# Optimization experiments

Hardware: AMD Instinct MI355X
Metric: run time of the kernel (lower is better)

The kernel has to match this reference:

```python
import jax, jax.numpy as jnp
import numpy as np

DIM = 512
NUM_HEADS = 8
B, NW, W = 8, 64, 64  # batch, num_windows, window_size


def setup_inputs() -> dict:
    key = jax.random.key(0)
    k1, k2, k3 = jax.random.split(key, 3)
    x = jax.random.normal(k1, (B, NW, W, DIM), dtype=jnp.float32)
    w_qkv = jax.random.normal(k2, (DIM, 3 * DIM), dtype=jnp.float32) * (DIM ** -0.5)
    w_proj = jax.random.normal(k3, (DIM, DIM), dtype=jnp.float32) * (DIM ** -0.5)
    b_proj = jnp.zeros((DIM,), dtype=jnp.float32)
    return {"x": x, "w_qkv": w_qkv, "w_proj": w_proj, "b_proj": b_proj}


def reference(x, w_qkv, w_proj, b_proj):
    batch, nw, w, dim = x.shape
    heads = NUM_HEADS
    dh = dim // heads
    scale = dh ** -0.5
    # qkv projection (no bias): [B, nW, W, 3*dim]
    qkv = jnp.einsum('bnwc,cd->bnwd', x, w_qkv)
    # -> [B, nW, W, 3, H, dh] -> [3, B, H, nW, W, dh]
    qkv = qkv.reshape(batch, nw, w, 3, heads, dh)
    qkv = jnp.transpose(qkv, (3, 0, 4, 1, 2, 5))
    q, k, v = qkv[0], qkv[1], qkv[2]
    # attention logits per window: [B, H, nW, W, W]
    attn = jnp.einsum('bhnqd,bhnkd->bhnqk', q, k) * scale
    attn = jax.nn.softmax(attn, axis=-1)
    # [B, H, nW, W, dh]
    out = jnp.einsum('bhnqk,bhnkd->bhnqd', attn, v)
    # faithful raw reshape (no transpose), matching the TF source
    out = out.reshape(batch, nw, w, dim)
    return jnp.einsum('bnwc,cd->bnwd', out, w_proj) + b_proj
```

## Files before the change

kernel.cpp:

```cpp
#include <hip/hip_runtime.h>
#include <hip/hip_bf16.h>

typedef __bf16 bf16_t;
typedef __bf16 bf16x8 __attribute__((ext_vector_type(8)));
typedef float f32x4 __attribute__((ext_vector_type(4)));

__global__ __launch_bounds__(256) void transpose_cast_kernel(
    const float* __restrict__ src, bf16_t* __restrict__ dst, int R, int C)
{
    __shared__ float tile[32][33];
    const int bx = blockIdx.x;
    const int by = blockIdx.y;
    const int t  = threadIdx.x;
    const int i0 = t >> 5;
    const int j  = t & 31;
#pragma unroll
    for (int p = 0; p < 4; ++p) {
        int i = i0 + p * 8;
        tile[i][j] = src[(long)(by * 32 + i) * C + bx * 32 + j];
    }
    __syncthreads();
#pragma unroll
    for (int p = 0; p < 4; ++p) {
        int i = i0 + p * 8;
        dst[(long)(bx * 32 + i) * R + by * 32 + j] = (bf16_t)tile[j][i];
    }
}

__global__ __launch_bounds__(256) void qkv_attn_kernel(
    const float*  __restrict__ x,
    const bf16_t* __restrict__ wT,
    bf16_t* __restrict__ ao)
{
    __shared__ bf16_t arena1[64 * 72];
    __shared__ bf16_t arena2[192 * 72];

    bf16_t* const lXc = arena1;
    bf16_t* const lP  = arena1;
    bf16_t* const lW  = arena2;
    bf16_t* const lQ  = arena2;
    bf16_t* const lK  = arena2 + 64 * 72;
    bf16_t* const lVT = arena2 + 128 * 72;

    const int id  = blockIdx.x;
    const int xcd = id & 7;
    const int s   = id >> 3;
    const int wid = xcd * 64 + (s >> 3);
    const int h   = s & 7;

    const int bb  = wid >> 6;
    const int nw  = wid & 63;
    const float* xw = x + (long)wid * 64 * 512;

    const int t    = threadIdx.x;
    const int wave = t >> 6;
    const int lane = t & 63;
    const int lr   = lane & 15;
    const int q    = lane >> 4;

    const float scale = 0.125f;

    f32x4 acc[12];
#pragma unroll
    for (int j = 0; j < 12; ++j) acc[j] = (f32x4)0.0f;

    for (int kc = 0; kc < 8; ++kc) {
        const int k0 = kc * 64;
#pragma unroll
        for (int p = 0; p < 2; ++p) {
            const int v = t + p * 256;
            const int r = v >> 3, c = (v & 7) * 8;
            const float* rp = xw + (long)r * 512 + k0 + c;
            f32x4 f0 = *(const f32x4*)rp;
            f32x4 f1 = *(const f32x4*)(rp + 4);
            bf16x8 o;
            o[0] = (bf16_t)f0[0]; o[1] = (bf16_t)f0[1];
            o[2] = (bf16_t)f0[2]; o[3] = (bf16_t)f0[3];
            o[4] = (bf16_t)f1[0]; o[5] = (bf16_t)f1[1];
            o[6] = (bf16_t)f1[2]; o[7] = (bf16_t)f1[3];
            *(bf16x8*)&lXc[r * 72 + c] = o;
        }
#pragma unroll
        for (int p = 0; p < 6; ++p) {
            const int v = t + p * 256;
            const int nr = v >> 3, c = (v & 7) * 8;
            const int g = nr >> 6, i = nr & 63;
            *(bf16x8*)&lW[nr * 72 + c] =
                *(const bf16x8*)(wT + (long)(g * 512 + h * 64 + i) * 512 + k0 + c);
        }
        __syncthreads();
#pragma unroll
        for (int ks = 0; ks < 64; ks += 32) {
            bf16x8 af = *(const bf16x8*)&lXc[(wave * 16 + lr) * 72 + ks + q * 8];
#pragma unroll
            for (int j = 0; j < 12; ++j) {
                bf16x8 bf = *(const bf16x8*)&lW[(j * 16 + lr) * 72 + ks + q * 8];
                acc[j] = __builtin_amdgcn_mfma_f32_16x16x32_bf16(af, bf, acc[j], 0, 0, 0);
            }
        }
        __syncthreads();
    }

#pragma unroll
    for (int j = 0; j < 4; ++j)
#pragma unroll
        for (int reg = 0; reg < 4; ++reg) {
            const int row = wave * 16 + q * 4 + reg;
            lQ[row * 72 + j * 16 + lr] = (bf16_t)acc[j][reg];
        }
#pragma unroll
    for (int j = 4; j < 8; ++j)
#pragma unroll
        for (int reg = 0; reg < 4; ++reg) {
            const int row = wave * 16 + q * 4 + reg;
            lK[row * 72 + (j - 4) * 16 + lr] = (bf16_t)acc[j][reg];
        }
#pragma unroll
    for (int j = 8; j < 12; ++j)
#pragma unroll
        for (int reg = 0; reg < 4; ++reg) {
            const int row = wave * 16 + q * 4 + reg;
            lVT[((j - 8) * 16 + lr) * 72 + row] = (bf16_t)acc[j][reg];
        }
    __syncthreads();

    f32x4 sAcc[4];
#pragma unroll
    for (int j = 0; j < 4; ++j) sAcc[j] = (f32x4)0.0f;
#pragma unroll
    for (int ks = 0; ks < 64; ks += 32) {
        bf16x8 aq = *(const bf16x8*)&lQ[(wave * 16 + lr) * 72 + ks + q * 8];
#pragma unroll
        for (int j = 0; j < 4; ++j) {
            bf16x8 bk = *(const bf16x8*)&lK[(j * 16 + lr) * 72 + ks + q * 8];
            sAcc[j] = __builtin_amdgcn_mfma_f32_16x16x32_bf16(aq, bk, sAcc[j], 0, 0, 0);
        }
    }

#pragma unroll
    for (int reg = 0; reg < 4; ++reg) {
        float m = fmaxf(fmaxf(sAcc[0][reg], sAcc[1][reg]),
                        fmaxf(sAcc[2][reg], sAcc[3][reg]));
#pragma unroll
        for (int d = 1; d < 16; d <<= 1) m = fmaxf(m, __shfl_xor(m, d));
        float p[4];
        float sum = 0.0f;
#pragma unroll
        for (int j = 0; j < 4; ++j) {
            p[j] = __expf((sAcc[j][reg] - m) * scale);
            sum += p[j];
        }
#pragma unroll
        for (int d = 1; d < 16; d <<= 1) sum += __shfl_xor(sum, d);
        const float inv = 1.0f / sum;
        const int row = wave * 16 + q * 4 + reg;
#pragma unroll
        for (int j = 0; j < 4; ++j)
            lP[row * 72 + j * 16 + lr] = (bf16_t)(p[j] * inv);
    }

    f32x4 o[4];
#pragma unroll
    for (int d4 = 0; d4 < 4; ++d4) o[d4] = (f32x4)0.0f;
#pragma unroll
    for (int ks = 0; ks < 64; ks += 32) {
        bf16x8 ap = *(const bf16x8*)&lP[(wave * 16 + lr) * 72 + ks + q * 8];
#pragma unroll
        for (int d4 = 0; d4 < 4; ++d4) {
            bf16x8 bv = *(const bf16x8*)&lVT[(d4 * 16 + lr) * 72 + ks + q * 8];
            o[d4] = __builtin_amdgcn_mfma_f32_16x16x32_bf16(ap, bv, o[d4], 0, 0, 0);
        }
    }

    bf16_t* aop = ao + ((long)bb * 4096 + (long)h * 512 + nw * 8) * 512;
#pragma unroll
    for (int d4 = 0; d4 < 4; ++d4)
#pragma unroll
        for (int reg = 0; reg < 4; ++reg) {
            const int wr = wave * 16 + q * 4 + reg;
            aop[(long)(wr >> 3) * 512 + (wr & 7) * 64 + d4 * 16 + lr] =
                (bf16_t)o[d4][reg];
        }
}

#define LDP 72

__global__ __launch_bounds__(256) void gemm2_kernel(
    const bf16_t* __restrict__ A,
    const bf16_t* __restrict__ Bt,
    const float*  __restrict__ bias,
    float* __restrict__ C,
    int M, int N, int K)
{
    __shared__ bf16_t lA[128 * LDP];
    __shared__ bf16_t lB[128 * LDP];

    const int tid  = threadIdx.x;
    const int wave = tid >> 6;
    const int lane = tid & 63;
    const int wm   = wave >> 1;
    const int wn   = wave & 1;
    const int lr   = lane & 15;
    const int q    = lane >> 4;

    const int id  = blockIdx.x;
    const int xcd = id & 7;
    const int s   = id >> 3;
    const int bm  = xcd * 32 + (s >> 2);
    const int bn  = s & 3;

    const long arow0 = (long)bm * 128;
    const long brow0 = (long)bn * 128;

    f32x4 acc[4][4];
#pragma unroll
    for (int i = 0; i < 4; ++i)
#pragma unroll
        for (int j = 0; j < 4; ++j) acc[i][j] = (f32x4)0.0f;

    const int srow = tid >> 3;
    const int scol = (tid & 7) * 8;

    const int nk = K / 64;
    for (int kt = 0; kt < nk; ++kt) {
        const bf16_t* Ag = A + arow0 * K + kt * 64;
        const bf16_t* Bg = Bt + brow0 * K + kt * 64;
        bf16x8 av[4], bv[4];
#pragma unroll
        for (int p = 0; p < 4; ++p) {
            const int r = srow + p * 32;
            av[p] = *(const bf16x8*)(Ag + (long)r * K + scol);
            bv[p] = *(const bf16x8*)(Bg + (long)r * K + scol);
        }
#pragma unroll
        for (int p = 0; p < 4; ++p) {
            const int r = srow + p * 32;
            *(bf16x8*)&lA[r * LDP + scol] = av[p];
            *(bf16x8*)&lB[r * LDP + scol] = bv[p];
        }
        __syncthreads();
#pragma unroll
        for (int ks = 0; ks < 64; ks += 32) {
            bf16x8 af[4], bf[4];
#pragma unroll
            for (int i = 0; i < 4; ++i)
                af[i] = *(const bf16x8*)&lA[(wm * 64 + i * 16 + lr) * LDP + ks + q * 8];
#pragma unroll
            for (int j = 0; j < 4; ++j)
                bf[j] = *(const bf16x8*)&lB[(wn * 64 + j * 16 + lr) * LDP + ks + q * 8];
#pragma unroll
            for (int i = 0; i < 4; ++i)
#pragma unroll
                for (int j = 0; j < 4; ++j)
                    acc[i][j] = __builtin_amdgcn_mfma_f32_16x16x32_bf16(
                        af[i], bf[j], acc[i][j], 0, 0, 0);
        }
        __syncthreads();
    }

#pragma unroll
    for (int i = 0; i < 4; ++i) {
        const long r = arow0 + wm * 64 + i * 16 + q * 4;
#pragma unroll
        for (int j = 0; j < 4; ++j) {
            const long c = brow0 + wn * 64 + j * 16 + lr;
            const float bv2 = bias[c];
#pragma unroll
            for (int reg = 0; reg < 4; ++reg) {
                C[(r + reg) * N + c] = acc[i][j][reg] + bv2;
            }
        }
    }
}

extern "C" void kernel_launch(void* const* d_in, const int* in_sizes, int n_in,
                              void* d_out, int out_size, void* d_ws, size_t ws_size,
                              hipStream_t stream)
{
    (void)in_sizes; (void)n_in; (void)out_size; (void)ws_size;
    const float* x     = (const float*)d_in[0];
    const float* wqkv  = (const float*)d_in[1];
    const float* wproj = (const float*)d_in[2];
    const float* bproj = (const float*)d_in[3];
    float* out = (float*)d_out;

    bf16_t* wT = (bf16_t*)d_ws;
    bf16_t* pT = wT + (size_t)1536 * 512;
    bf16_t* ao = pT + (size_t)512 * 512;

    transpose_cast_kernel<<<dim3(48, 16), 256, 0, stream>>>(wqkv, wT, 512, 1536);
    transpose_cast_kernel<<<dim3(16, 16), 256, 0, stream>>>(wproj, pT, 512, 512);

    qkv_attn_kernel<<<4096, 256, 0, stream>>>(x, wT, ao);

    gemm2_kernel<<<1024, 256, 0, stream>>>(
        ao, pT, bproj, out, 32768, 512, 512);
}
```

Before: 228.9 us.

## Process two windows per block with 2x2 wave tiling and pre-cast x to bf16

Each block of the fused QKV+attention kernel now handles two windows (128 rows) instead of one, with waves arranged 2x2 so each wave computes a 64x96 sub-tile of the QKV projection. This reuses each loaded weight tile across twice as many rows, halving weight traffic per window. x is cast to bf16 once by a separate elementwise kernel, so the fused kernel loads bf16 directly. LDS padding is removed (stride 64), which may add bank conflicts. The extra cast pass adds a full read and write of x, and launch bounds now request 3 blocks per CU.

```diff
diff --git a/kernel.cpp b/kernel.cpp
--- a/kernel.cpp
+++ b/kernel.cpp
@@ -27,160 +27,201 @@
     }
 }
 
-__global__ __launch_bounds__(256) void qkv_attn_kernel(
-    const float*  __restrict__ x,
+__global__ __launch_bounds__(256) void cast_bf16_kernel(
+    const float* __restrict__ src, bf16_t* __restrict__ dst, long n)
+{
+    const long i = ((long)blockIdx.x * 256 + threadIdx.x) * 8;
+    if (i < n) {
+        f32x4 a = *(const f32x4*)(src + i);
+        f32x4 b = *(const f32x4*)(src + i + 4);
+        bf16x8 o;
+        o[0] = (bf16_t)a[0]; o[1] = (bf16_t)a[1];
+        o[2] = (bf16_t)a[2]; o[3] = (bf16_t)a[3];
+        o[4] = (bf16_t)b[0]; o[5] = (bf16_t)b[1];
+        o[6] = (bf16_t)b[2]; o[7] = (bf16_t)b[3];
+        *(bf16x8*)(dst + i) = o;
+    }
+}
+
+__global__ __launch_bounds__(256, 3) void qkv_attn_kernel(
+    const bf16_t* __restrict__ xb,
     const bf16_t* __restrict__ wT,
     bf16_t* __restrict__ ao)
 {
-    __shared__ bf16_t arena1[64 * 72];
-    __shared__ bf16_t arena2[192 * 72];
-
-    bf16_t* const lXc = arena1;
-    bf16_t* const lP  = arena1;
-    bf16_t* const lW  = arena2;
-    bf16_t* const lQ  = arena2;
-    bf16_t* const lK  = arena2 + 64 * 72;
-    bf16_t* const lVT = arena2 + 128 * 72;
-
-    const int id  = blockIdx.x;
-    const int xcd = id & 7;
-    const int s   = id >> 3;
-    const int wid = xcd * 64 + (s >> 3);
-    const int h   = s & 7;
-
-    const int bb  = wid >> 6;
-    const int nw  = wid & 63;
-    const float* xw = x + (long)wid * 64 * 512;
+    __shared__ bf16_t lds[24576];
+    bf16_t* const lX = lds;
+    bf16_t* const lW = lds + 8192;
+
+    const int id   = blockIdx.x;
+    const int xcd  = id & 7;
+    const int s    = id >> 3;
+    const int pair = xcd * 32 + (s >> 3);
+    const int h    = s & 7;
 
     const int t    = threadIdx.x;
     const int wave = t >> 6;
     const int lane = t & 63;
     const int lr   = lane & 15;
     const int q    = lane >> 4;
+    const int wm   = wave >> 1;
+    const int wn   = wave & 1;
+
+    const bf16_t* xw = xb + (long)pair * 128 * 512;
 
     const float scale = 0.125f;
 
-    f32x4 acc[12];
-#pragma unroll
-    for (int j = 0; j < 12; ++j) acc[j] = (f32x4)0.0f;
+    f32x4 acc[4][6];
+#pragma unroll
+    for (int i = 0; i < 4; ++i)
+#pragma unroll
+        for (int j = 0; j < 6; ++j) acc[i][j] = (f32x4)0.0f;
 
     for (int kc = 0; kc < 8; ++kc) {
         const int k0 = kc * 64;
 #pragma unroll
-        for (int p = 0; p < 2; ++p) {
+        for (int p = 0; p < 4; ++p) {
             const int v = t + p * 256;
             const int r = v >> 3, c = (v & 7) * 8;
-            const float* rp = xw + (long)r * 512 + k0 + c;
-            f32x4 f0 = *(const f32x4*)rp;
-            f32x4 f1 = *(const f32x4*)(rp + 4);
-            bf16x8 o;
-            o[0] = (bf16_t)f0[0]; o[1] = (bf16_t)f0[1];
-            o[2] = (bf16_t)f0[2]; o[3] = (bf16_t)f0[3];
-            o[4] = (bf16_t)f1[0]; o[5] = (bf16_t)f1[1];
-            o[6] = (bf16_t)f1[2]; o[7] = (bf16_t)f1[3];
-            *(bf16x8*)&lXc[r * 72 + c] = o;
+            *(bf16x8*)&lX[r * 64 + c] = *(const bf16x8*)(xw + (long)r * 512 + k0 + c);
         }
 #pragma unroll
         for (int p = 0; p < 6; ++p) {
             const int v = t + p * 256;
             const int nr = v >> 3, c = (v & 7) * 8;
             const int g = nr >> 6, i = nr & 63;
-            *(bf16x8*)&lW[nr * 72 + c] =
+            *(bf16x8*)&lW[nr * 64 + c] =
                 *(const bf16x8*)(wT + (long)(g * 512 + h * 64 + i) * 512 + k0 + c);
         }
         __syncthreads();
 #pragma unroll
         for (int ks = 0; ks < 64; ks += 32) {
-            bf16x8 af = *(const bf16x8*)&lXc[(wave * 16 + lr) * 72 + ks + q * 8];
-#pragma unroll
-            for (int j = 0; j < 12; ++j) {
-                bf16x8 bf = *(const bf16x8*)&lW[(j * 16 + lr) * 72 + ks + q * 8];
-                acc[j] = __builtin_amdgcn_mfma_f32_16x16x32_bf16(af, bf, acc[j], 0, 0, 0);
+            bf16x8 af[4], bf[6];
+#pragma unroll
+            for (int i = 0; i < 4; ++i)
+                af[i] = *(const bf16x8*)&lX[(wm * 64 + i * 16 + lr) * 64 + ks + q * 8];
+#pragma unroll
+            for (int j = 0; j < 6; ++j)
+                bf[j] = *(const bf16x8*)&lW[(wn * 96 + j * 16 + lr) * 64 + ks + q * 8];
+#pragma unroll
+            for (int i = 0; i < 4; ++i)
+#pragma unroll
+                for (int j = 0; j < 6; ++j)
+                    acc[i][j] = __builtin_amdgcn_mfma_f32_16x16x32_bf16(
+                        af[i], bf[j], acc[i][j], 0, 0, 0);
+        }
+        __syncthreads();
+    }
+
+    {
+        bf16_t* const tQ  = &lds[wm * 12288];
+        bf16_t* const tK  = tQ + 4096;
+        bf16_t* const tVT = tQ + 8192;
+#pragma unroll
+        for (int i = 0; i < 4; ++i)
+#pragma unroll
+            for (int j = 0; j < 6; ++j) {
+                const int col = wn * 96 + j * 16 + lr;
+#pragma unroll
+                for (int reg = 0; reg < 4; ++reg) {
+                    const int wr = i * 16 + q * 4 + reg;
+                    const bf16_t val = (bf16_t)acc[i][j][reg];
+                    if (col < 64)       tQ[wr * 64 + col];
+                    if (col < 64)       tQ[wr * 64 + col] = val;
+                    else if (col < 128) tK[wr * 64 + (col - 64)] = val;
+                    else                tVT[(col - 128) * 64 + wr] = val;
+                }
             }
-        }
-        __syncthreads();
-    }
-
-#pragma unroll
-    for (int j = 0; j < 4; ++j)
+    }
+    __syncthreads();
+
+    const int wv   = wave >> 1;
+    const int half = wave & 1;
+    bf16_t* const tQ  = &lds[wv * 12288];
+    bf16_t* const tK  = tQ + 4096;
+    bf16_t* const tVT = tQ + 8192;
+
+    f32x4 sA[2][4];
+#pragma unroll
+    for (int rt = 0; rt < 2; ++rt)
+#pragma unroll
+        for (int j = 0; j < 4; ++j) sA[rt][j] = (f32x4)0.0f;
+#pragma unroll
+    for (int ks = 0; ks < 64; ks += 32) {
+        bf16x8 aq[2], bk[4];
+#pragma unroll
+        for (int rt = 0; rt < 2; ++rt)
+            aq[rt] = *(const bf16x8*)&tQ[(half * 32 + rt * 16 + lr) * 64 + ks + q * 8];
+#pragma unroll
+        for (int j = 0; j < 4; ++j)
+            bk[j] = *(const bf16x8*)&tK[(j * 16 + lr) * 64 + ks + q * 8];
+#pragma unroll
+        for (int rt = 0; rt < 2; ++rt)
+#pragma unroll
+            for (int j = 0; j < 4; ++j)
+                sA[rt][j] = __builtin_amdgcn_mfma_f32_16x16x32_bf16(
+                    aq[rt], bk[j], sA[rt][j], 0, 0, 0);
+    }
+
+#pragma unroll
+    for (int rt = 0; rt < 2; ++rt)
 #pragma unroll
         for (int reg = 0; reg < 4; ++reg) {
-            const int row = wave * 16 + q * 4 + reg;
-            lQ[row * 72 + j * 16 + lr] = (bf16_t)acc[j][reg];
-        }
-#pragma unroll
-    for (int j = 4; j < 8; ++j)
-#pragma unroll
-        for (int reg = 0; reg < 4; ++reg) {
-            const int row = wave * 16 + q * 4 + reg;
-            lK[row * 72 + (j - 4) * 16 + lr] = (bf16_t)acc[j][reg];
-        }
-#pragma unroll
-    for (int j = 8; j < 12; ++j)
-#pragma unroll
-        for (int reg = 0; reg < 4; ++reg) {
-            const int row = wave * 16 + q * 4 + reg;
-            lVT[((j - 8) * 16 + lr) * 72 + row] = (bf16_t)acc[j][reg];
-        }
-    __syncthreads();
-
-    f32x4 sAcc[4];
-#pragma unroll
-    for (int j = 0; j < 4; ++j) sAcc[j] = (f32x4)0.0f;
+            float m = fmaxf(fmaxf(sA[rt][0][reg], sA[rt][1][reg]),
+                            fmaxf(sA[rt][2][reg], sA[rt][3][reg]));
+#pragma unroll
+            for (int d = 1; d < 16; d <<= 1) m = fmaxf(m, __shfl_xor(m, d));
+            float p[4];
+            float sum = 0.0f;
+#pragma unroll
+            for (int j = 0; j < 4; ++j) {
+                p[j] = __expf((sA[rt][j][reg] - m) * scale);
+                sum += p[j];
+            }
+#pragma unroll
+            for (int d = 1; d < 16; d <<= 1) sum += __shfl_xor(sum, d);
+            const float inv = 1.0f / sum;
+            const int row = half * 32 + rt * 16 + q * 4 + reg;
+#pragma unroll
+            for (int j = 0; j < 4; ++j)
+                tQ[row * 64 + j * 16 + lr] = (bf16_t)(p[j] * inv);
+        }
+
+    f32x4 o[2][4];
+#pragma unroll
+    for (int rt = 0; rt < 2; ++rt)
+#pragma unroll
+        for (int d4 = 0; d4 < 4; ++d4) o[rt][d4] = (f32x4)0.0f;
 #pragma unroll
     for (int ks = 0; ks < 64; ks += 32) {
-        bf16x8 aq = *(const bf16x8*)&lQ[(wave * 16 + lr) * 72 + ks + q * 8];
-#pragma unroll
-        for (int j = 0; j < 4; ++j) {
-            bf16x8 bk = *(const bf16x8*)&lK[(j * 16 + lr) * 72 + ks + q * 8];
-            sAcc[j] = __builtin_amdgcn_mfma_f32_16x16x32_bf16(aq, bk, sAcc[j], 0, 0, 0);
-        }
-    }
-
-#pragma unroll
-    for (int reg = 0; reg < 4; ++reg) {
-        float m = fmaxf(fmaxf(sAcc[0][reg], sAcc[1][reg]),
-                        fmaxf(sAcc[2][reg], sAcc[3][reg]));
-#pragma unroll
-        for (int d = 1; d < 16; d <<= 1) m = fmaxf(m, __shfl_xor(m, d));
-        float p[4];
-        float sum = 0.0f;
-#pragma unroll
-        for (int j = 0; j < 4; ++j) {
-            p[j] = __expf((sAcc[j][reg] - m) * scale);
-            sum += p[j];
-        }
-#pragma unroll
-        for (int d = 1; d < 16; d <<= 1) sum += __shfl_xor(sum, d);
-        const float inv = 1.0f / sum;
-        const int row = wave * 16 + q * 4 + reg;
-#pragma unroll
-        for (int j = 0; j < 4; ++j)
-            lP[row * 72 + j * 16 + lr] = (bf16_t)(p[j] * inv);
-    }
-
-    f32x4 o[4];
-#pragma unroll
-    for (int d4 = 0; d4 < 4; ++d4) o[d4] = (f32x4)0.0f;
-#pragma unroll
-    for (int ks = 0; ks < 64; ks += 32) {
-        bf16x8 ap = *(const bf16x8*)&lP[(wave * 16 + lr) * 72 + ks + q * 8];
-#pragma unroll
-        for (int d4 = 0; d4 < 4; ++d4) {
-            bf16x8 bv = *(const bf16x8*)&lVT[(d4 * 16 + lr) * 72 + ks + q * 8];
-            o[d4] = __builtin_amdgcn_mfma_f32_16x16x32_bf16(ap, bv, o[d4], 0, 0, 0);
-        }
-    }
-
+        bf16x8 ap[2], bv[4];
+#pragma unroll
+        for (int rt = 0; rt < 2; ++rt)
+            ap[rt] = *(const bf16x8*)&tQ[(half * 32 + rt * 16 + lr) * 64 + ks + q * 8];
+#pragma unroll
+        for (int d4 = 0; d4 < 4; ++d4)
+            bv[d4] = *(const bf16x8*)&tVT[(d4 * 16 + lr) * 64 + ks + q * 8];
+#pragma unroll
+        for (int rt = 0; rt < 2; ++rt)
+#pragma unroll
+            for (int d4 = 0; d4 < 4; ++d4)
+                o[rt][d4] = __builtin_amdgcn_mfma_f32_16x16x32_bf16(
+                    ap[rt], bv[d4], o[rt][d4], 0, 0, 0);
+    }
+
+    const int wid = pair * 2 + wv;
+    const int bb  = wid >> 6;
+    const int nw  = wid & 63;
     bf16_t* aop = ao + ((long)bb * 4096 + (long)h * 512 + nw * 8) * 512;
 #pragma unroll
-    for (int d4 = 0; d4 < 4; ++d4)
-#pragma unroll
-        for (int reg = 0; reg < 4; ++reg) {
-            const int wr = wave * 16 + q * 4 + reg;
-            aop[(long)(wr >> 3) * 512 + (wr & 7) * 64 + d4 * 16 + lr] =
-                (bf16_t)o[d4][reg];
-        }
+    for (int rt = 0; rt < 2; ++rt)
+#pragma unroll
+        for (int d4 = 0; d4 < 4; ++d4)
+#pragma unroll
+            for (int reg = 0; reg < 4; ++reg) {
+                const int wr = half * 32 + rt * 16 + q * 4 + reg;
+                aop[(long)(wr >> 3) * 512 + (wr & 7) * 64 + d4 * 16 + lr] =
+                    (bf16_t)o[rt][d4][reg];
+            }
 }
 
 #define LDP 72
@@ -287,11 +328,15 @@
     bf16_t* wT = (bf16_t*)d_ws;
     bf16_t* pT = wT + (size_t)1536 * 512;
     bf16_t* ao = pT + (size_t)512 * 512;
+    bf16_t* xb = ao + (size_t)32768 * 512;
 
     transpose_cast_kernel<<<dim3(48, 16), 256, 0, stream>>>(wqkv, wT, 512, 1536);
     transpose_cast_kernel<<<dim3(16, 16), 256, 0, stream>>>(wproj, pT, 512, 512);
 
-    qkv_attn_kernel<<<4096, 256, 0, stream>>>(x, wT, ao);
+    const long nx = (long)16777216;
+    cast_bf16_kernel<<<(int)(nx / 2048), 256, 0, stream>>>(x, xb, nx);
+
+    qkv_attn_kernel<<<2048, 256, 0, stream>>>(xb, wT, ao);
 
     gemm2_kernel<<<1024, 256, 0, stream>>>(
         ao, pT, bproj, out, 32768, 512, 512);
```

Measured after the change: 239.1 us. +4.5%, slower.
